# Kernel optimization log

Measured on AMD Instinct MI355X. Metric: run time of the kernel, lower is better.

The kernel has to match this reference:

```python
import jax, jax.numpy as jnp
from jax import lax
import numpy as np

V, E, H, B, L = 50000, 100, 512, 1024, 128


def _gru_params(key, E, H, dtype=jnp.float32):
    k = 1.0 / np.sqrt(H)
    ks = jax.random.split(key, 4)
    Wih = jax.random.uniform(ks[0], (3 * H, E), dtype, -k, k)
    Whh = jax.random.uniform(ks[1], (3 * H, H), dtype, -k, k)
    bih = jax.random.uniform(ks[2], (3 * H,), dtype, -k, k)
    bhh = jax.random.uniform(ks[3], (3 * H,), dtype, -k, k)
    return Wih, Whh, bih, bhh


def setup_inputs() -> dict:
    key = jax.random.key(0)
    kc, kr, kec, ker, kgc, kgr = jax.random.split(key, 6)
    contexts = jax.random.randint(kc, (B, L), 0, V)
    replies = jax.random.randint(kr, (B, L), 0, V)
    ctx_emb = jax.random.uniform(kec, (V, E), jnp.float32, -0.25, 0.25)
    rep_emb = jax.random.uniform(ker, (V, E), jnp.float32, -0.25, 0.25)
    ctx_Wih, ctx_Whh, ctx_bih, ctx_bhh = _gru_params(kgc, E, H)
    rep_Wih, rep_Whh, rep_bih, rep_bhh = _gru_params(kgr, E, H)
    return dict(contexts=contexts, replies=replies,
                ctx_emb=ctx_emb, ctx_Wih=ctx_Wih, ctx_Whh=ctx_Whh, ctx_bih=ctx_bih, ctx_bhh=ctx_bhh,
                rep_emb=rep_emb, rep_Wih=rep_Wih, rep_Whh=rep_Whh, rep_bih=rep_bih, rep_bhh=rep_bhh)


def _gru_backward_last(x, Wih, Whh, bih, bhh):
    """Final hidden of the backward direction of a bidirectional GRU.
    x: [B, L, E] -> h: [B, H]. enc_h_t[-1] in torch == reverse-direction final state,
    i.e. a GRU run over the time-reversed sequence."""
    Bsz = x.shape[0]
    Hh = Whh.shape[1]
    xs = jnp.swapaxes(x, 0, 1)[::-1]  # [L, B, E], reversed time

    def step(h, xt):
        gi = xt @ Wih.T + bih          # [B, 3H]
        gh = h @ Whh.T + bhh           # [B, 3H]
        i_r, i_z, i_n = jnp.split(gi, 3, axis=-1)
        h_r, h_z, h_n = jnp.split(gh, 3, axis=-1)
        r = jax.nn.sigmoid(i_r + h_r)
        z = jax.nn.sigmoid(i_z + h_z)
        n = jnp.tanh(i_n + r * h_n)
        h_new = (1.0 - z) * n + z * h
        return h_new, None

    h0 = jnp.zeros((Bsz, Hh), x.dtype)
    h_last, _ = lax.scan(step, h0, xs)
    return h_last


def reference(contexts, replies,
              ctx_emb, ctx_Wih, ctx_Whh, ctx_bih, ctx_bhh,
              rep_emb, rep_Wih, rep_Whh, rep_bih, rep_bhh):
    # embedding lookup (dropout is identity at eval)
    ex_c = ctx_emb[contexts]  # [B, L, E]
    ex_r = rep_emb[replies]   # [B, L, E]
    hc = _gru_backward_last(ex_c, ctx_Wih, ctx_Whh, ctx_bih, ctx_bhh)  # [B, H]
    hr = _gru_backward_last(ex_r, rep_Wih, rep_Whh, rep_bih, rep_bhh)  # [B, H]
    # fused equivalent of the nested-loop per-pair dot products + row softmax
    scores = hc @ hr.T  # [B, B]
    return jax.nn.softmax(scores, axis=-1)
```

## Files before the change

### kernel.cpp

```cpp
#include <hip/hip_runtime.h>
#include <math.h>

#define B_SZ   1024
#define H_SZ   512
#define E_SZ   100
#define L_SZ   128
#define KX     128
#define VOCAB  50000

typedef _Float16 f16x8 __attribute__((ext_vector_type(8)));
typedef float    f32x4 __attribute__((ext_vector_type(4)));

#define MFMA16(a, b, c) __builtin_amdgcn_mfma_f32_16x16x32_f16((a), (b), (c), 0, 0, 0)

__device__ __forceinline__ float fast_sigmoid(float x) {
    return __builtin_amdgcn_rcpf(1.0f + __expf(-x));
}
__device__ __forceinline__ float fast_tanh(float x) {
    return 1.0f - 2.0f * __builtin_amdgcn_rcpf(1.0f + __expf(2.0f * x));
}

__global__ __launch_bounds__(256) void prep_emb_kernel(
    _Float16* __restrict__ ef_c, const float* __restrict__ e_c,
    _Float16* __restrict__ ef_r, const float* __restrict__ e_r)
{
    const int PER = VOCAB * KX;
    int idx = blockIdx.x * 256 + threadIdx.x;
    if (idx >= 2 * PER) return;
    const int gru = idx >= PER;
    const int local = gru ? idx - PER : idx;
    const int v = local >> 7;
    const int e = local & 127;
    const float* src = gru ? e_r : e_c;
    _Float16* dst = gru ? ef_r : ef_c;
    dst[local] = (_Float16)(e < E_SZ ? src[v * E_SZ + e] : 0.0f);
}

struct GruArgs {
    const float* Whh[2];
    const float* Wih[2];
    const float* bih[2];
    const float* bhh[2];
    const _Float16* emb[2];
    const int* idx[2];
    _Float16* hA;
    _Float16* hB;
    unsigned int* bars;
    unsigned int* claim;
};

__global__ __launch_bounds__(512, 2) void gru_persistent(GruArgs args)
{
    __shared__ int role_s;
    if (threadIdx.x == 0) {
        unsigned xcd;
        asm volatile("s_getreg_b32 %0, hwreg(HW_REG_XCC_ID)" : "=s"(xcd));
        xcd &= 7u;
        unsigned slot = atomicAdd(&args.claim[xcd], 1u);
        role_s = (int)(xcd * 32u + slot);
    }
    __syncthreads();
    const int role = role_s;
    const int grp  = role >> 4;
    const int ut   = role & 15;
    const int gru  = grp >> 3;
    const int mt   = grp & 7;

    const float* __restrict__ Whh = args.Whh[gru];
    const float* __restrict__ Wih = args.Wih[gru];
    const float* __restrict__ bih = args.bih[gru];
    const float* __restrict__ bhh = args.bhh[gru];
    const _Float16* __restrict__ embf = args.emb[gru];
    const int* __restrict__ idx = args.idx[gru];

    const int u0 = ut * 32;
    const int mB = mt * 128;

    __shared__ _Float16 Wl[7680 * 8];

    for (int f = threadIdx.x; f < 7680; f += 512) {
        const int ln  = f & 63;
        const int q   = f >> 6;
        const int kc  = q / 6;
        const int rem = q - kc * 6;
        const int g   = rem >> 1;
        const int u2  = rem & 1;
        const int row = g * H_SZ + u0 + u2 * 16 + (ln & 15);
        const int ks  = ln >> 4;
        _Float16 tmp[8];
        if (kc < 16) {
            const float* src = Whh + (size_t)row * H_SZ + kc * 32 + ks * 8;
#pragma unroll
            for (int j = 0; j < 8; ++j) tmp[j] = (_Float16)src[j];
        } else {
            const int e = (kc - 16) * 32 + ks * 8;
#pragma unroll
            for (int j = 0; j < 8; ++j)
                tmp[j] = (_Float16)((e + j < E_SZ) ? Wih[(size_t)row * E_SZ + e + j]
                                                   : 0.0f);
        }
        *(f16x8*)&Wl[(size_t)f * 8] = *(const f16x8*)tmp;
    }
    __syncthreads();

    const int lane = threadIdx.x & 63;
    const int wave = threadIdx.x >> 6;
    const int lr   = lane & 15;
    const int kseg = lane >> 4;
    const int mw   = mB + wave * 16;

    const _Float16* Wbase = Wl + (size_t)lane * 8;
#define WFRAG(kc, g, u2) \
    (*(const f16x8*)(Wbase + (size_t)((((kc) * 3 + (g)) * 2 + (u2)) * 64) * 8))

    float bir[2], biz[2], binn[2], bhn[2];
    int ucol[2];
#pragma unroll
    for (int u2 = 0; u2 < 2; ++u2) {
        ucol[u2] = u0 + u2 * 16 + lr;
        const int u = ucol[u2];
        bir[u2]  = bih[u]             + bhh[u];
        biz[u2]  = bih[H_SZ + u]      + bhh[H_SZ + u];
        binn[u2] = bih[2 * H_SZ + u];
        bhn[u2]  = bhh[2 * H_SZ + u];
    }

    _Float16* hbuf0 = args.hA + (size_t)gru * B_SZ * H_SZ;
    _Float16* hbuf1 = args.hB + (size_t)gru * B_SZ * H_SZ;
    unsigned int* bar = args.bars + grp * 32;

    float hreg[2][4] = {};

    f16x8 er0, er1, er2, er3;
    int ivn;
    {
        const int iv_c = idx[(mw + lr) * L_SZ + (L_SZ - 1)];
        const _Float16* e0 = embf + (size_t)iv_c * KX + kseg * 8;
        er0 = *(const f16x8*)(e0);
        er1 = *(const f16x8*)(e0 + 32);
        er2 = *(const f16x8*)(e0 + 64);
        er3 = *(const f16x8*)(e0 + 96);
        ivn = idx[(mw + lr) * L_SZ + (L_SZ - 2)];
    }

#pragma unroll 1
    for (int step = 0; step < L_SZ; ++step) {
        const _Float16* __restrict__ hin = (step & 1) ? hbuf1 : hbuf0;
        _Float16* __restrict__ hout      = (step & 1) ? hbuf0 : hbuf1;

        f32x4 accr[2], accz[2], acchn[2], accin[2];
#pragma unroll
        for (int j = 0; j < 2; j++) {
            accr[j]  = (f32x4){0.f, 0.f, 0.f, 0.f};
            accz[j]  = (f32x4){0.f, 0.f, 0.f, 0.f};
            acchn[j] = (f32x4){0.f, 0.f, 0.f, 0.f};
            accin[j] = (f32x4){0.f, 0.f, 0.f, 0.f};
        }

#pragma unroll
        for (int xc = 0; xc < 4; ++xc) {
            const f16x8 ea = (xc == 0) ? er0 : (xc == 1) ? er1
                           : (xc == 2) ? er2 : er3;
#pragma unroll
            for (int u2 = 0; u2 < 2; ++u2) {
                f16x8 b0 = WFRAG(16 + xc, 0, u2);
                f16x8 b1 = WFRAG(16 + xc, 1, u2);
                f16x8 b2 = WFRAG(16 + xc, 2, u2);
                accr[u2]  = MFMA16(ea, b0, accr[u2]);
                accz[u2]  = MFMA16(ea, b1, accz[u2]);
                accin[u2] = MFMA16(ea, b2, accin[u2]);
            }
        }

        if (step > 0) {
            if (threadIdx.x == 0) {
                const unsigned tgt = 16u * (unsigned)step;
                while (__hip_atomic_load(bar, __ATOMIC_RELAXED,
                                         __HIP_MEMORY_SCOPE_AGENT) < tgt)
                    __builtin_amdgcn_s_sleep(1);
            }
            __syncthreads();
        }

        const _Float16* hrow0 = hin + (mw + lr) * H_SZ + kseg * 8;
        f16x8 a0h[16];
        asm volatile(
            "global_load_dwordx4 %0,  %16, off sc0\n\t"
            "global_load_dwordx4 %1,  %16, off offset:64 sc0\n\t"
            "global_load_dwordx4 %2,  %16, off offset:128 sc0\n\t"
            "global_load_dwordx4 %3,  %16, off offset:192 sc0\n\t"
            "global_load_dwordx4 %4,  %16, off offset:256 sc0\n\t"
            "global_load_dwordx4 %5,  %16, off offset:320 sc0\n\t"
            "global_load_dwordx4 %6,  %16, off offset:384 sc0\n\t"
            "global_load_dwordx4 %7,  %16, off offset:448 sc0\n\t"
            "global_load_dwordx4 %8,  %16, off offset:512 sc0\n\t"
            "global_load_dwordx4 %9,  %16, off offset:576 sc0\n\t"
            "global_load_dwordx4 %10, %16, off offset:640 sc0\n\t"
            "global_load_dwordx4 %11, %16, off offset:704 sc0\n\t"
            "global_load_dwordx4 %12, %16, off offset:768 sc0\n\t"
            "global_load_dwordx4 %13, %16, off offset:832 sc0\n\t"
            "global_load_dwordx4 %14, %16, off offset:896 sc0\n\t"
            "global_load_dwordx4 %15, %16, off offset:960 sc0\n\t"
            "s_waitcnt vmcnt(0)"
            : "=&v"(a0h[0]),  "=&v"(a0h[1]),  "=&v"(a0h[2]),  "=&v"(a0h[3]),
              "=&v"(a0h[4]),  "=&v"(a0h[5]),  "=&v"(a0h[6]),  "=&v"(a0h[7]),
              "=&v"(a0h[8]),  "=&v"(a0h[9]),  "=&v"(a0h[10]), "=&v"(a0h[11]),
              "=&v"(a0h[12]), "=&v"(a0h[13]), "=&v"(a0h[14]), "=&v"(a0h[15])
            : "v"(hrow0)
            : "memory");

        {
            const _Float16* erow = embf + (size_t)ivn * KX + kseg * 8;
            er0 = *(const f16x8*)(erow);
            er1 = *(const f16x8*)(erow + 32);
            er2 = *(const f16x8*)(erow + 64);
            er3 = *(const f16x8*)(erow + 96);
            int lc = L_SZ - 3 - step;
            if (lc < 0) lc = 0;
            ivn = idx[(mw + lr) * L_SZ + lc];
        }

#pragma unroll
        for (int kc = 0; kc < 16; ++kc) {
#pragma unroll
            for (int u2 = 0; u2 < 2; ++u2) {
                f16x8 b0 = WFRAG(kc, 0, u2);
                f16x8 b1 = WFRAG(kc, 1, u2);
                f16x8 b2 = WFRAG(kc, 2, u2);
                accr[u2]  = MFMA16(a0h[kc], b0, accr[u2]);
                accz[u2]  = MFMA16(a0h[kc], b1, accz[u2]);
                acchn[u2] = MFMA16(a0h[kc], b2, acchn[u2]);
            }
        }

#pragma unroll
        for (int u2 = 0; u2 < 2; ++u2) {
#pragma unroll
            for (int r = 0; r < 4; ++r) {
                const int m = mw + kseg * 4 + r;
                const float rg = fast_sigmoid(accr[u2][r] + bir[u2]);
                const float zg = fast_sigmoid(accz[u2][r] + biz[u2]);
                const float ng = fast_tanh(accin[u2][r] + binn[u2] +
                                           rg * (acchn[u2][r] + bhn[u2]));
                float nh = (1.0f - zg) * ng + zg * hreg[u2][r];
                nh = (float)(_Float16)nh;
                hreg[u2][r] = nh;
                hout[m * H_SZ + ucol[u2]] = (_Float16)nh;
            }
        }

        if (step + 1 < L_SZ) {
            __syncthreads();
            if (threadIdx.x == 0) {
                __hip_atomic_fetch_add(bar, 1u, __ATOMIC_RELAXED,
                                       __HIP_MEMORY_SCOPE_AGENT);
            }
        }
    }
#undef WFRAG
}

__global__ __launch_bounds__(256, 1) void scores_kernel(
    const _Float16* __restrict__ hc, const _Float16* __restrict__ hr,
    float* __restrict__ out)
{
    const int lane = threadIdx.x & 63;
    const int wave = threadIdx.x >> 6;
    const int lr   = lane & 15;
    const int kseg = lane >> 4;
    const int m0 = blockIdx.y * 64 + (wave >> 1) * 32;
    const int n0 = blockIdx.x * 64 + (wave & 1) * 32;

    f32x4 acc[2][2];
#pragma unroll
    for (int i = 0; i < 2; i++)
#pragma unroll
        for (int j = 0; j < 2; j++)
            acc[i][j] = (f32x4){0.f, 0.f, 0.f, 0.f};

#pragma unroll 2
    for (int kc = 0; kc < 16; kc++) {
        const int k0 = kc * 32 + kseg * 8;
        f16x8 a[2], b[2];
#pragma unroll
        for (int mt = 0; mt < 2; mt++)
            a[mt] = *(const f16x8*)(hc + (m0 + mt * 16 + lr) * H_SZ + k0);
#pragma unroll
        for (int nt = 0; nt < 2; nt++)
            b[nt] = *(const f16x8*)(hr + (n0 + nt * 16 + lr) * H_SZ + k0);
#pragma unroll
        for (int mt = 0; mt < 2; mt++)
#pragma unroll
            for (int nt = 0; nt < 2; nt++)
                acc[mt][nt] = MFMA16(a[mt], b[nt], acc[mt][nt]);
    }

#pragma unroll
    for (int mt = 0; mt < 2; mt++)
#pragma unroll
        for (int nt = 0; nt < 2; nt++)
#pragma unroll
            for (int r = 0; r < 4; r++) {
                const int m = m0 + mt * 16 + kseg * 4 + r;
                const int n = n0 + nt * 16 + lr;
                out[m * B_SZ + n] = acc[mt][nt][r];
            }
}

__global__ __launch_bounds__(256) void softmax_kernel(float* __restrict__ out)
{
    const int row = blockIdx.x;
    float* p = out + (size_t)row * B_SZ;
    const int t = threadIdx.x;
    const int wave = t >> 6;
    const int lane = t & 63;

    float4 v = ((const float4*)p)[t];
    float m = fmaxf(fmaxf(v.x, v.y), fmaxf(v.z, v.w));
#pragma unroll
    for (int off = 32; off >= 1; off >>= 1)
        m = fmaxf(m, __shfl_xor(m, off, 64));

    __shared__ float redm[4];
    if (lane == 0) redm[wave] = m;
    __syncthreads();
    m = fmaxf(fmaxf(redm[0], redm[1]), fmaxf(redm[2], redm[3]));

    const float e0 = __expf(v.x - m);
    const float e1 = __expf(v.y - m);
    const float e2 = __expf(v.z - m);
    const float e3 = __expf(v.w - m);
    float s = e0 + e1 + e2 + e3;
#pragma unroll
    for (int off = 32; off >= 1; off >>= 1)
        s += __shfl_xor(s, off, 64);

    __shared__ float reds[4];
    if (lane == 0) reds[wave] = s;
    __syncthreads();
    s = reds[0] + reds[1] + reds[2] + reds[3];

    const float inv = 1.0f / s;
    float4 o;
    o.x = e0 * inv; o.y = e1 * inv; o.z = e2 * inv; o.w = e3 * inv;
    ((float4*)p)[t] = o;
}

extern "C" void kernel_launch(void* const* d_in, const int* in_sizes, int n_in,
                              void* d_out, int out_size, void* d_ws, size_t ws_size,
                              hipStream_t stream)
{
    (void)in_sizes; (void)n_in; (void)out_size; (void)ws_size;

    const int*   contexts = (const int*)d_in[0];
    const int*   replies  = (const int*)d_in[1];
    const float* ctx_emb  = (const float*)d_in[2];
    const float* ctx_Wih  = (const float*)d_in[3];
    const float* ctx_Whh  = (const float*)d_in[4];
    const float* ctx_bih  = (const float*)d_in[5];
    const float* ctx_bhh  = (const float*)d_in[6];
    const float* rep_emb  = (const float*)d_in[7];
    const float* rep_Wih  = (const float*)d_in[8];
    const float* rep_Whh  = (const float*)d_in[9];
    const float* rep_bih  = (const float*)d_in[10];
    const float* rep_bhh  = (const float*)d_in[11];
    float* out = (float*)d_out;

    const size_t EMB_ELEMS = (size_t)VOCAB * KX;
    const size_t H_ELEMS   = (size_t)B_SZ * H_SZ;

    _Float16* base   = (_Float16*)d_ws;
    _Float16* embf_c = base;
    _Float16* embf_r = embf_c + EMB_ELEMS;
    _Float16* hB     = embf_r + EMB_ELEMS;
    _Float16* hA     = hB + 2 * H_ELEMS;
    unsigned int* bars  = (unsigned int*)(hA + 2 * H_ELEMS);
    unsigned int* claim = bars + 16 * 32;

    hipMemsetAsync(hA, 0,
                   2 * H_ELEMS * sizeof(_Float16) +
                   (16 * 32 + 8) * sizeof(unsigned int), stream);

    {
        const int total_emb = 2 * (int)EMB_ELEMS;
        prep_emb_kernel<<<(total_emb + 255) / 256, 256, 0, stream>>>(
            embf_c, ctx_emb, embf_r, rep_emb);
    }

    GruArgs a;
    a.Whh[0] = ctx_Whh; a.Whh[1] = rep_Whh;
    a.Wih[0] = ctx_Wih; a.Wih[1] = rep_Wih;
    a.bih[0] = ctx_bih; a.bih[1] = rep_bih;
    a.bhh[0] = ctx_bhh; a.bhh[1] = rep_bhh;
    a.emb[0] = embf_c;  a.emb[1] = embf_r;
    a.idx[0] = contexts; a.idx[1] = replies;
    a.hA = hA; a.hB = hB; a.bars = bars; a.claim = claim;
    gru_persistent<<<dim3(256), dim3(512), 0, stream>>>(a);

    scores_kernel<<<dim3(B_SZ / 64, B_SZ / 64), 256, 0, stream>>>(hA, hA + H_ELEMS, out);
    softmax_kernel<<<B_SZ, 256, 0, stream>>>(out);
}
```

Before: 1.006 ms.

## Split GRU hidden units across twice as many persistent blocks

Doubles the persistent GRU grid from 256 to 512 blocks. Each block now owns 16 hidden units instead of 32, which halves the per-block LDS weight slice and the MFMA work per step. The role mapping is reworked so the two batch groups on each XCD interleave, and the barrier target is raised to 32 arrivals per group. In exchange, every block reloads the full hidden row each step and more blocks must sync at each barrier. It also requires 4 blocks of 512 threads to be co-resident per CU, or the persistent barrier could deadlock.

```diff
diff --git a/kernel.cpp b/kernel.cpp
--- a/kernel.cpp
+++ b/kernel.cpp
@@ -49,7 +49,7 @@
     unsigned int* claim;
 };
 
-__global__ __launch_bounds__(512, 2) void gru_persistent(GruArgs args)
+__global__ __launch_bounds__(512, 4) void gru_persistent(GruArgs args)
 {
     __shared__ int role_s;
     if (threadIdx.x == 0) {
@@ -57,12 +57,14 @@
         asm volatile("s_getreg_b32 %0, hwreg(HW_REG_XCC_ID)" : "=s"(xcd));
         xcd &= 7u;
         unsigned slot = atomicAdd(&args.claim[xcd], 1u);
-        role_s = (int)(xcd * 32u + slot);
+        role_s = (int)(xcd * 64u + slot);
     }
     __syncthreads();
     const int role = role_s;
-    const int grp  = role >> 4;
-    const int ut   = role & 15;
+    const int xcd  = role >> 6;
+    const int slot = role & 63;
+    const int grp  = xcd * 2 + (slot & 1);
+    const int ut   = slot >> 1;
     const int gru  = grp >> 3;
     const int mt   = grp & 7;
 
@@ -73,19 +75,17 @@
     const _Float16* __restrict__ embf = args.emb[gru];
     const int* __restrict__ idx = args.idx[gru];
 
-    const int u0 = ut * 32;
+    const int u0 = ut * 16;
     const int mB = mt * 128;
 
-    __shared__ _Float16 Wl[7680 * 8];
-
-    for (int f = threadIdx.x; f < 7680; f += 512) {
+    __shared__ _Float16 Wl[3840 * 8];
+
+    for (int f = threadIdx.x; f < 3840; f += 512) {
         const int ln  = f & 63;
         const int q   = f >> 6;
-        const int kc  = q / 6;
-        const int rem = q - kc * 6;
-        const int g   = rem >> 1;
-        const int u2  = rem & 1;
-        const int row = g * H_SZ + u0 + u2 * 16 + (ln & 15);
+        const int kc  = q / 3;
+        const int g   = q - kc * 3;
+        const int row = g * H_SZ + u0 + (ln & 15);
         const int ks  = ln >> 4;
         _Float16 tmp[8];
         if (kc < 16) {
@@ -110,26 +110,20 @@
     const int mw   = mB + wave * 16;
 
     const _Float16* Wbase = Wl + (size_t)lane * 8;
-#define WFRAG(kc, g, u2) \
-    (*(const f16x8*)(Wbase + (size_t)((((kc) * 3 + (g)) * 2 + (u2)) * 64) * 8))
-
-    float bir[2], biz[2], binn[2], bhn[2];
-    int ucol[2];
-#pragma unroll
-    for (int u2 = 0; u2 < 2; ++u2) {
-        ucol[u2] = u0 + u2 * 16 + lr;
-        const int u = ucol[u2];
-        bir[u2]  = bih[u]             + bhh[u];
-        biz[u2]  = bih[H_SZ + u]      + bhh[H_SZ + u];
-        binn[u2] = bih[2 * H_SZ + u];
-        bhn[u2]  = bhh[2 * H_SZ + u];
-    }
+#define WFRAG(kc, g) \
+    (*(const f16x8*)(Wbase + (size_t)(((kc) * 3 + (g)) * 64) * 8))
+
+    const int ucol = u0 + lr;
+    const float bir  = bih[ucol]            + bhh[ucol];
+    const float biz  = bih[H_SZ + ucol]     + bhh[H_SZ + ucol];
+    const float binn = bih[2 * H_SZ + ucol];
+    const float bhn  = bhh[2 * H_SZ + ucol];
 
     _Float16* hbuf0 = args.hA + (size_t)gru * B_SZ * H_SZ;
     _Float16* hbuf1 = args.hB + (size_t)gru * B_SZ * H_SZ;
     unsigned int* bar = args.bars + grp * 32;
 
-    float hreg[2][4] = {};
+    float hreg[4] = {};
 
     f16x8 er0, er1, er2, er3;
     int ivn;
@@ -148,33 +142,23 @@
         const _Float16* __restrict__ hin = (step & 1) ? hbuf1 : hbuf0;
         _Float16* __restrict__ hout      = (step & 1) ? hbuf0 : hbuf1;
 
-        f32x4 accr[2], accz[2], acchn[2], accin[2];
-#pragma unroll
-        for (int j = 0; j < 2; j++) {
-            accr[j]  = (f32x4){0.f, 0.f, 0.f, 0.f};
-            accz[j]  = (f32x4){0.f, 0.f, 0.f, 0.f};
-            acchn[j] = (f32x4){0.f, 0.f, 0.f, 0.f};
-            accin[j] = (f32x4){0.f, 0.f, 0.f, 0.f};
-        }
+        f32x4 accr  = (f32x4){0.f, 0.f, 0.f, 0.f};
+        f32x4 accz  = (f32x4){0.f, 0.f, 0.f, 0.f};
+        f32x4 acchn = (f32x4){0.f, 0.f, 0.f, 0.f};
+        f32x4 accin = (f32x4){0.f, 0.f, 0.f, 0.f};
 
 #pragma unroll
         for (int xc = 0; xc < 4; ++xc) {
             const f16x8 ea = (xc == 0) ? er0 : (xc == 1) ? er1
                            : (xc == 2) ? er2 : er3;
-#pragma unroll
-            for (int u2 = 0; u2 < 2; ++u2) {
-                f16x8 b0 = WFRAG(16 + xc, 0, u2);
-                f16x8 b1 = WFRAG(16 + xc, 1, u2);
-                f16x8 b2 = WFRAG(16 + xc, 2, u2);
-                accr[u2]  = MFMA16(ea, b0, accr[u2]);
-                accz[u2]  = MFMA16(ea, b1, accz[u2]);
-                accin[u2] = MFMA16(ea, b2, accin[u2]);
-            }
+            accr  = MFMA16(ea, WFRAG(16 + xc, 0), accr);
+            accz  = MFMA16(ea, WFRAG(16 + xc, 1), accz);
+            accin = MFMA16(ea, WFRAG(16 + xc, 2), accin);
         }
 
         if (step > 0) {
             if (threadIdx.x == 0) {
-                const unsigned tgt = 16u * (unsigned)step;
+                const unsigned tgt = 32u * (unsigned)step;
                 while (__hip_atomic_load(bar, __ATOMIC_RELAXED,
                                          __HIP_MEMORY_SCOPE_AGENT) < tgt)
                     __builtin_amdgcn_s_sleep(1);
@@ -222,31 +206,22 @@
 
 #pragma unroll
         for (int kc = 0; kc < 16; ++kc) {
-#pragma unroll
-            for (int u2 = 0; u2 < 2; ++u2) {
-                f16x8 b0 = WFRAG(kc, 0, u2);
-                f16x8 b1 = WFRAG(kc, 1, u2);
-                f16x8 b2 = WFRAG(kc, 2, u2);
-                accr[u2]  = MFMA16(a0h[kc], b0, accr[u2]);
-                accz[u2]  = MFMA16(a0h[kc], b1, accz[u2]);
-                acchn[u2] = MFMA16(a0h[kc], b2, acchn[u2]);
-            }
-        }
-
-#pragma unroll
-        for (int u2 = 0; u2 < 2; ++u2) {
-#pragma unroll
-            for (int r = 0; r < 4; ++r) {
-                const int m = mw + kseg * 4 + r;
-                const float rg = fast_sigmoid(accr[u2][r] + bir[u2]);
-                const float zg = fast_sigmoid(accz[u2][r] + biz[u2]);
-                const float ng = fast_tanh(accin[u2][r] + binn[u2] +
-                                           rg * (acchn[u2][r] + bhn[u2]));
-                float nh = (1.0f - zg) * ng + zg * hreg[u2][r];
-                nh = (float)(_Float16)nh;
-                hreg[u2][r] = nh;
-                hout[m * H_SZ + ucol[u2]] = (_Float16)nh;
-            }
+            accr  = MFMA16(a0h[kc], WFRAG(kc, 0), accr);
+            accz  = MFMA16(a0h[kc], WFRAG(kc, 1), accz);
+            acchn = MFMA16(a0h[kc], WFRAG(kc, 2), acchn);
+        }
+
+#pragma unroll
+        for (int r = 0; r < 4; ++r) {
+            const int m = mw + kseg * 4 + r;
+            const float rg = fast_sigmoid(accr[r] + bir);
+            const float zg = fast_sigmoid(accz[r] + biz);
+            const float ng = fast_tanh(accin[r] + binn +
+                                       rg * (acchn[r] + bhn));
+            float nh = (1.0f - zg) * ng + zg * hreg[r];
+            nh = (float)(_Float16)nh;
+            hreg[r] = nh;
+            hout[m * H_SZ + ucol] = (_Float16)nh;
         }
 
         if (step + 1 < L_SZ) {
@@ -257,6 +232,7 @@
             }
         }
     }
+    asm volatile("s_waitcnt vmcnt(0)" ::: "memory");
 #undef WFRAG
 }
 
@@ -395,7 +371,7 @@
     a.emb[0] = embf_c;  a.emb[1] = embf_r;
     a.idx[0] = contexts; a.idx[1] = replies;
     a.hA = hA; a.hB = hB; a.bars = bars; a.claim = claim;
-    gru_persistent<<<dim3(256), dim3(512), 0, stream>>>(a);
+    gru_persistent<<<dim3(512), dim3(512), 0, stream>>>(a);
 
     scores_kernel<<<dim3(B_SZ / 64, B_SZ / 64), 256, 0, stream>>>(hA, hA + H_ELEMS, out);
     softmax_kernel<<<B_SZ, 256, 0, stream>>>(out);
```

Measured after the change: 1.751 ms. 74.1% more time.
